# Optimization experiments

Measured on AMD Instinct MI355X. Metric: run time of the kernel, lower is better.

The kernel has to match this reference:

```python
import jax, jax.numpy as jnp
import numpy as np

ALPHA = 1.0
BETA = 10.0
OHEM_RATIO = 3
EPS = 1e-7  # clamp for BCE logs (torch BCELoss clamps log at -100; EPS keeps it finite)


def setup_inputs() -> dict:
    key = jax.random.key(0)
    k1, k2, k3, k4 = jax.random.split(key, 4)
    B, H, W = 16, 640, 640
    # channel 0 is a probability map (fed to BCELoss directly) -> uniform (0,1)
    outputs = jax.random.uniform(k1, (B, 3, H, W), dtype=jnp.float32)
    gt_shrink_labels = jax.random.bernoulli(k2, 0.05, (B, H, W)).astype(jnp.float32)
    # border threshold map in [0,1], mostly zero
    gt_threshold_labels = (jax.random.uniform(k3, (B, H, W), dtype=jnp.float32)
                           * jax.random.bernoulli(k4, 0.1, (B, H, W)).astype(jnp.float32))
    return {
        "outputs": outputs,
        "gt_shrink_labels": gt_shrink_labels,
        "gt_threshold_labels": gt_threshold_labels,
    }


def _ohem_mask(score, gt):
    """Per-sample OHEM: keep all positives + top (pos_num*ratio) hardest negatives.
    score, gt: [H, W]. Returns float mask [H, W]. Mirrors ohem_single exactly."""
    n = score.size
    pos = gt > 0.5
    pos_num = jnp.sum(pos)
    neg_cnt = n - pos_num
    neg_num = jnp.minimum(pos_num * OHEM_RATIO, neg_cnt)
    # negatives only, sorted descending (positives pushed to the bottom)
    neg_scores = jnp.where(pos.ravel(), -jnp.inf, score.ravel())
    sorted_desc = -jnp.sort(-neg_scores)
    idx = jnp.clip(neg_num - 1, 0, n - 1)
    thr = sorted_desc[idx]
    sel = ((score >= thr) | pos).astype(score.dtype)
    all_ones = (pos_num == 0) | (neg_num == 0)
    return jnp.where(all_ones, jnp.ones_like(score), sel)


def _masked_bce(p, t, m):
    """Mean BCE over masked pixels (= torch BCELoss on the selected subset)."""
    p = jnp.clip(p, EPS, 1.0 - EPS)
    l = -(t * jnp.log(p) + (1.0 - t) * jnp.log1p(-p))
    s = jnp.sum(m)
    return jnp.where(s > 0, jnp.sum(l * m) / jnp.maximum(s, 1.0), 0.0)


def _bce_loss(prob, gt):
    mask = jax.lax.stop_gradient(_ohem_mask(prob, gt))  # torch uses .data (detached)
    return _masked_bce(prob, gt, mask)


def _threshold_loss(thr_map, gt_thr, gt_shrink):
    sel = ((gt_thr > 0) | (gt_shrink > 0)).astype(thr_map.dtype)
    s = jnp.sum(sel)
    l1 = jnp.sum(jnp.abs(thr_map - gt_thr) * sel)
    return jnp.where(s > 0, l1 / jnp.maximum(s, 1.0), 0.0)


def _per_sample(shrink_map, threshold_map, binary_map, gt_shrink, gt_thr):
    loss_shrink = _bce_loss(shrink_map, gt_shrink)
    loss_binary = _bce_loss(jax.nn.sigmoid(binary_map), gt_shrink)
    loss_threshold = _threshold_loss(threshold_map, gt_thr, gt_shrink)
    return loss_shrink, loss_binary, loss_threshold


def reference(outputs, gt_shrink_labels, gt_threshold_labels):
    shrink_maps = outputs[:, 0, :, :]
    threshold_maps = outputs[:, 1, :, :]
    binary_maps = outputs[:, 2, :, :]
    ls, lb, lt = jax.vmap(_per_sample)(shrink_maps, threshold_maps, binary_maps,
                                       gt_shrink_labels, gt_threshold_labels)
    # reduction == 'mean'
    loss_shrink = jnp.mean(ls)
    loss_binary = jnp.mean(lb)
    loss_threshold = jnp.mean(lt)
    loss_all = loss_shrink + ALPHA * loss_binary + BETA * loss_threshold
    return (loss_all, loss_shrink, loss_binary, loss_threshold)
```

## Files before the change

kernel.cpp:

```cpp
#include <hip/hip_runtime.h>
#include <math.h>
#include <stddef.h>

#define BATCH 16
#define NPIX (640 * 640)
#define NBIN 512
#define FIXS 4096.0f

struct WS {
  float posNum[BATCH];
  float posLossS[BATCH];
  float posLossB[BATCH];
  float selCnt[BATCH];
  float l1Sum[BATCH];
  float lsPart[BATCH];
  float lbPart[BATCH];
  unsigned hcnt[2][BATCH][NBIN];
  unsigned hsum[2][BATCH][NBIN];
};

__device__ __forceinline__ int bucketOf(float x) {
  int b = (int)(x * (float)NBIN);
  return b < 0 ? 0 : (b > NBIN - 1 ? NBIN - 1 : b);
}

__device__ __forceinline__ float blockSum(float v, volatile float* lds4) {
#pragma unroll
  for (int o = 32; o > 0; o >>= 1) v += __shfl_down(v, o, 64);
  int lane = threadIdx.x & 63, w = threadIdx.x >> 6;
  __syncthreads();
  if (lane == 0) lds4[w] = v;
  __syncthreads();
  return lds4[0] + lds4[1] + lds4[2] + lds4[3];
}

__global__ void __launch_bounds__(256) k_main(const float* __restrict__ out4,
                                              const float* __restrict__ gts,
                                              const float* __restrict__ gtt,
                                              WS* ws) {
  const int s = blockIdx.y;
  __shared__ unsigned hc0[NBIN], hc1[NBIN];
  __shared__ float hs0[NBIN], hs1[NBIN];
  for (int i = threadIdx.x; i < NBIN; i += 256) {
    hc0[i] = 0u; hc1[i] = 0u; hs0[i] = 0.f; hs1[i] = 0.f;
  }
  __syncthreads();

  const float4* p0 = (const float4*)(out4 + ((size_t)s * 3 + 0) * NPIX);
  const float4* p1 = (const float4*)(out4 + ((size_t)s * 3 + 1) * NPIX);
  const float4* p2 = (const float4*)(out4 + ((size_t)s * 3 + 2) * NPIX);
  const float4* g = (const float4*)(gts + (size_t)s * NPIX);
  const float4* t = (const float4*)(gtt + (size_t)s * NPIX);
  const int n4 = NPIX / 4;
  const float lo = 1e-7f, hi = 1.0f - 1e-7f;

  float posC = 0.f, pls = 0.f, plb = 0.f, sel = 0.f, l1 = 0.f;

  auto procPix = [&](const float4& gv, const float4& tv, const float4& a0,
                     const float4& a1, const float4& a2) {
    float ga[4] = {gv.x, gv.y, gv.z, gv.w};
    float ta[4] = {tv.x, tv.y, tv.z, tv.w};
    float x0[4] = {a0.x, a0.y, a0.z, a0.w};
    float x1[4] = {a1.x, a1.y, a1.z, a1.w};
    float x2[4] = {a2.x, a2.y, a2.z, a2.w};
#pragma unroll
    for (int j = 0; j < 4; ++j) {
      const float tt = ga[j];
      if (ta[j] > 0.f || tt > 0.f) {
        sel += 1.f;
        l1 += fabsf(x1[j] - ta[j]);
      }
      float p = fminf(fmaxf(x0[j], lo), hi);
      float l0 = -(tt * __logf(p) + (1.f - tt) * __logf(1.f - p));
      float sg = 1.f / (1.f + __expf(-x2[j]));
      float q = fminf(fmaxf(sg, lo), hi);
      float l2 = -(tt * __logf(q) + (1.f - tt) * __logf(1.f - q));
      if (tt > 0.5f) {
        posC += 1.f; pls += l0; plb += l2;
      } else {
        atomicAdd(&hc0[bucketOf(x0[j])], 1u);
        atomicAdd(&hs0[bucketOf(x0[j])], l0);
        atomicAdd(&hc1[bucketOf(x2[j])], 1u);
        atomicAdd(&hs1[bucketOf(x2[j])], l2);
      }
    }
  };

  const int stride = gridDim.x * 256;
  int i = blockIdx.x * 256 + threadIdx.x;
  for (; i + stride < n4; i += 2 * stride) {
    float4 gvA = g[i], tvA = t[i], a0A = p0[i], a1A = p1[i], a2A = p2[i];
    int i2 = i + stride;
    float4 gvB = g[i2], tvB = t[i2], a0B = p0[i2], a1B = p1[i2], a2B = p2[i2];
    procPix(gvA, tvA, a0A, a1A, a2A);
    procPix(gvB, tvB, a0B, a1B, a2B);
  }
  if (i < n4) {
    float4 gvA = g[i], tvA = t[i], a0A = p0[i], a1A = p1[i], a2A = p2[i];
    procPix(gvA, tvA, a0A, a1A, a2A);
  }
  __syncthreads();

  for (int b = threadIdx.x; b < NBIN; b += 256) {
    unsigned c = hc0[b];
    if (c) atomicAdd(&ws->hcnt[0][s][b], c);
    unsigned u = (unsigned)__float2uint_rn(hs0[b] * FIXS);
    if (u) atomicAdd(&ws->hsum[0][s][b], u);
    c = hc1[b];
    if (c) atomicAdd(&ws->hcnt[1][s][b], c);
    u = (unsigned)__float2uint_rn(hs1[b] * FIXS);
    if (u) atomicAdd(&ws->hsum[1][s][b], u);
  }

  __shared__ float lds4[4];
  float r;
  r = blockSum(posC, lds4);
  if (threadIdx.x == 0) atomicAdd(&ws->posNum[s], r);
  r = blockSum(pls, lds4);
  if (threadIdx.x == 0) atomicAdd(&ws->posLossS[s], r);
  r = blockSum(plb, lds4);
  if (threadIdx.x == 0) atomicAdd(&ws->posLossB[s], r);
  r = blockSum(sel, lds4);
  if (threadIdx.x == 0) atomicAdd(&ws->selCnt[s], r);
  r = blockSum(l1, lds4);
  if (threadIdx.x == 0) atomicAdd(&ws->l1Sum[s], r);
}

__global__ void __launch_bounds__(256) k_fin(WS* ws) {
  const int ty = blockIdx.x, s = blockIdx.y;
  const int tid = threadIdx.x;
  __shared__ float sc[256], sl[256];
  __shared__ float meanS;

  const unsigned* hc = ws->hcnt[ty][s];
  const unsigned* hs = ws->hsum[ty][s];
  const float pos = ws->posNum[s];
  const float posLoss = ty ? ws->posLossB[s] : ws->posLossS[s];
  const float negc = (float)NPIX - pos;
  const float k = fminf(3.f * pos, negc);

  const int base = tid * 2;
  const float c0 = (float)hc[base], c1 = (float)hc[base + 1];
  const float s0 = (float)hs[base] * (1.0f / FIXS);
  const float s1 = (float)hs[base + 1] * (1.0f / FIXS);
  sc[tid] = c0 + c1;
  sl[tid] = s0 + s1;
  __syncthreads();
  for (int off = 1; off < 256; off <<= 1) {
    float ac = (tid + off < 256) ? sc[tid + off] : 0.f;
    float al = (tid + off < 256) ? sl[tid + off] : 0.f;
    __syncthreads();
    sc[tid] += ac;
    sl[tid] += al;
    __syncthreads();
  }
  if (k < 0.5f) {
    if (tid == 0) meanS = (posLoss + sl[0]) / (float)NPIX;
  } else {
    const float cumT = sc[tid];
    const float cumN = (tid < 255) ? sc[tid + 1] : 0.f;
    const float slN = (tid < 255) ? sl[tid + 1] : 0.f;
    if (cumT >= k && cumN < k) {
      float C_above, nb, bsum, S_above;
      if (cumN + c1 >= k) {
        C_above = cumN; nb = c1; bsum = s1; S_above = slN;
      } else {
        C_above = cumN + c1; nb = c0; bsum = s0; S_above = slN + s1;
      }
      const float krem = k - C_above;
      const float maskCnt = pos + C_above + krem;
      const float lossSum = posLoss + S_above + bsum * (krem / nb);
      meanS = lossSum / fmaxf(maskCnt, 1.f);
    }
  }
  __syncthreads();
  if (tid == 0) {
    if (ty) ws->lbPart[s] = meanS;
    else    ws->lsPart[s] = meanS;
  }
}

__global__ void k_out(const WS* __restrict__ ws, float* __restrict__ out) {
  if (threadIdx.x == 0) {
    float ls = 0.f, lb = 0.f, lt = 0.f;
    for (int s = 0; s < BATCH; ++s) {
      ls += ws->lsPart[s];
      lb += ws->lbPart[s];
      float sc = ws->selCnt[s];
      lt += (sc > 0.f) ? ws->l1Sum[s] / fmaxf(sc, 1.f) : 0.f;
    }
    ls /= (float)BATCH;
    lb /= (float)BATCH;
    lt /= (float)BATCH;
    out[0] = ls + 1.0f * lb + 10.0f * lt;
    out[1] = ls;
    out[2] = lb;
    out[3] = lt;
  }
}

extern "C" void kernel_launch(void* const* d_in, const int* in_sizes, int n_in,
                              void* d_out, int out_size, void* d_ws,
                              size_t ws_size, hipStream_t stream) {
  const float* out4 = (const float*)d_in[0];
  const float* gts = (const float*)d_in[1];
  const float* gtt = (const float*)d_in[2];
  WS* ws = (WS*)d_ws;

  hipMemsetAsync(d_ws, 0, sizeof(WS), stream);

  k_main<<<dim3(64, BATCH), dim3(256), 0, stream>>>(out4, gts, gtt, ws);
  k_fin<<<dim3(2, BATCH), dim3(256), 0, stream>>>(ws);
  k_out<<<1, 64, 0, stream>>>(ws, (float*)d_out);
}
```

Measured before the change: 199.8 us.

## Pack histogram count and fixed-point loss into one 64-bit LDS atomic

Replaces the two pairs of 32-bit shared-memory atomics (count plus float loss sum per histogram) with a single 64-bit atomic whose high word holds the count and low word the fixed-point loss. BCE is simplified to a single log per channel, using log(1+exp(±x)) in place of sigmoid followed by log. The load loop becomes a software-pipelined prefetch, and the grid is doubled to 128 blocks per sample. The aim is to halve LDS atomic traffic and cut transcendental work. In exchange, per-pixel rounding to fixed point and the 32-bit low word risk carry overflow into the count field for large bins, and the sigmoid loss is no longer clamped at EPS.

```diff
diff --git a/kernel.cpp b/kernel.cpp
--- a/kernel.cpp
+++ b/kernel.cpp
@@ -15,8 +15,7 @@
   float l1Sum[BATCH];
   float lsPart[BATCH];
   float lbPart[BATCH];
-  unsigned hcnt[2][BATCH][NBIN];
-  unsigned hsum[2][BATCH][NBIN];
+  unsigned long long hist[2][BATCH][NBIN];
 };
 
 __device__ __forceinline__ int bucketOf(float x) {
@@ -39,11 +38,8 @@
                                               const float* __restrict__ gtt,
                                               WS* ws) {
   const int s = blockIdx.y;
-  __shared__ unsigned hc0[NBIN], hc1[NBIN];
-  __shared__ float hs0[NBIN], hs1[NBIN];
-  for (int i = threadIdx.x; i < NBIN; i += 256) {
-    hc0[i] = 0u; hc1[i] = 0u; hs0[i] = 0.f; hs1[i] = 0.f;
-  }
+  __shared__ unsigned long long h0[NBIN], h1[NBIN];
+  for (int i = threadIdx.x; i < NBIN; i += 256) { h0[i] = 0ull; h1[i] = 0ull; }
   __syncthreads();
 
   const float4* p0 = (const float4*)(out4 + ((size_t)s * 3 + 0) * NPIX);
@@ -56,60 +52,62 @@
 
   float posC = 0.f, pls = 0.f, plb = 0.f, sel = 0.f, l1 = 0.f;
 
-  auto procPix = [&](const float4& gv, const float4& tv, const float4& a0,
-                     const float4& a1, const float4& a2) {
+  auto proc = [&](const float4& gv, const float4& tv, const float4& a1,
+                  const float4& a0, const float4& a2) {
     float ga[4] = {gv.x, gv.y, gv.z, gv.w};
     float ta[4] = {tv.x, tv.y, tv.z, tv.w};
-    float x0[4] = {a0.x, a0.y, a0.z, a0.w};
-    float x1[4] = {a1.x, a1.y, a1.z, a1.w};
-    float x2[4] = {a2.x, a2.y, a2.z, a2.w};
+    float y1[4] = {a1.x, a1.y, a1.z, a1.w};
+    float y0[4] = {a0.x, a0.y, a0.z, a0.w};
+    float y2[4] = {a2.x, a2.y, a2.z, a2.w};
 #pragma unroll
     for (int j = 0; j < 4; ++j) {
       const float tt = ga[j];
+      const bool posp = tt > 0.5f;
       if (ta[j] > 0.f || tt > 0.f) {
         sel += 1.f;
-        l1 += fabsf(x1[j] - ta[j]);
-      }
-      float p = fminf(fmaxf(x0[j], lo), hi);
-      float l0 = -(tt * __logf(p) + (1.f - tt) * __logf(1.f - p));
-      float sg = 1.f / (1.f + __expf(-x2[j]));
-      float q = fminf(fmaxf(sg, lo), hi);
-      float l2 = -(tt * __logf(q) + (1.f - tt) * __logf(1.f - q));
-      if (tt > 0.5f) {
+        l1 += fabsf(y1[j] - ta[j]);
+      }
+      const float p = fminf(fmaxf(y0[j], lo), hi);
+      const float l0 = -__logf(posp ? p : 1.f - p);
+      const float xb = y2[j];
+      const float l2 = __logf(1.f + __expf(posp ? -xb : xb));
+      if (posp) {
         posC += 1.f; pls += l0; plb += l2;
       } else {
-        atomicAdd(&hc0[bucketOf(x0[j])], 1u);
-        atomicAdd(&hs0[bucketOf(x0[j])], l0);
-        atomicAdd(&hc1[bucketOf(x2[j])], 1u);
-        atomicAdd(&hs1[bucketOf(x2[j])], l2);
+        unsigned long long pk0 =
+            (1ull << 32) | (unsigned long long)__float2uint_rn(l0 * FIXS);
+        unsigned long long pk1 =
+            (1ull << 32) | (unsigned long long)__float2uint_rn(l2 * FIXS);
+        atomicAdd(&h0[bucketOf(y0[j])], pk0);
+        atomicAdd(&h1[bucketOf(xb)], pk1);
       }
     }
   };
 
   const int stride = gridDim.x * 256;
   int i = blockIdx.x * 256 + threadIdx.x;
-  for (; i + stride < n4; i += 2 * stride) {
-    float4 gvA = g[i], tvA = t[i], a0A = p0[i], a1A = p1[i], a2A = p2[i];
-    int i2 = i + stride;
-    float4 gvB = g[i2], tvB = t[i2], a0B = p0[i2], a1B = p1[i2], a2B = p2[i2];
-    procPix(gvA, tvA, a0A, a1A, a2A);
-    procPix(gvB, tvB, a0B, a1B, a2B);
-  }
   if (i < n4) {
-    float4 gvA = g[i], tvA = t[i], a0A = p0[i], a1A = p1[i], a2A = p2[i];
-    procPix(gvA, tvA, a0A, a1A, a2A);
+    float4 gv = g[i], tv = t[i], a1 = p1[i], a0 = p0[i], a2 = p2[i];
+    for (;;) {
+      const int nx = i + stride;
+      if (nx < n4) {
+        float4 gv2 = g[nx], tv2 = t[nx], b1 = p1[nx], b0 = p0[nx], b2 = p2[nx];
+        proc(gv, tv, a1, a0, a2);
+        gv = gv2; tv = tv2; a1 = b1; a0 = b0; a2 = b2;
+        i = nx;
+      } else {
+        proc(gv, tv, a1, a0, a2);
+        break;
+      }
+    }
   }
   __syncthreads();
 
   for (int b = threadIdx.x; b < NBIN; b += 256) {
-    unsigned c = hc0[b];
-    if (c) atomicAdd(&ws->hcnt[0][s][b], c);
-    unsigned u = (unsigned)__float2uint_rn(hs0[b] * FIXS);
-    if (u) atomicAdd(&ws->hsum[0][s][b], u);
-    c = hc1[b];
-    if (c) atomicAdd(&ws->hcnt[1][s][b], c);
-    u = (unsigned)__float2uint_rn(hs1[b] * FIXS);
-    if (u) atomicAdd(&ws->hsum[1][s][b], u);
+    unsigned long long v = h0[b];
+    if (v) atomicAdd(&ws->hist[0][s][b], v);
+    v = h1[b];
+    if (v) atomicAdd(&ws->hist[1][s][b], v);
   }
 
   __shared__ float lds4[4];
@@ -132,17 +130,18 @@
   __shared__ float sc[256], sl[256];
   __shared__ float meanS;
 
-  const unsigned* hc = ws->hcnt[ty][s];
-  const unsigned* hs = ws->hsum[ty][s];
+  const unsigned long long* hh = ws->hist[ty][s];
   const float pos = ws->posNum[s];
   const float posLoss = ty ? ws->posLossB[s] : ws->posLossS[s];
   const float negc = (float)NPIX - pos;
   const float k = fminf(3.f * pos, negc);
 
   const int base = tid * 2;
-  const float c0 = (float)hc[base], c1 = (float)hc[base + 1];
-  const float s0 = (float)hs[base] * (1.0f / FIXS);
-  const float s1 = (float)hs[base + 1] * (1.0f / FIXS);
+  const unsigned long long v0 = hh[base], v1 = hh[base + 1];
+  const float c0 = (float)(unsigned)(v0 >> 32);
+  const float c1 = (float)(unsigned)(v1 >> 32);
+  const float s0 = (float)(unsigned)(v0 & 0xffffffffu) * (1.0f / FIXS);
+  const float s1 = (float)(unsigned)(v1 & 0xffffffffu) * (1.0f / FIXS);
   sc[tid] = c0 + c1;
   sl[tid] = s0 + s1;
   __syncthreads();
@@ -209,7 +208,7 @@
 
   hipMemsetAsync(d_ws, 0, sizeof(WS), stream);
 
-  k_main<<<dim3(64, BATCH), dim3(256), 0, stream>>>(out4, gts, gtt, ws);
+  k_main<<<dim3(128, BATCH), dim3(256), 0, stream>>>(out4, gts, gtt, ws);
   k_fin<<<dim3(2, BATCH), dim3(256), 0, stream>>>(ws);
   k_out<<<1, 64, 0, stream>>>(ws, (float*)d_out);
 }
```

Measured after the change: 200.0 us. About the same (+0.1%).
